# Optimization experiments

Hardware: AMD Instinct MI355X
Metric: run time of the kernel (lower is better)

## Reference

```python
import jax, jax.numpy as jnp
import numpy as np

N = 50000   # num_nodes
F = 128     # node_features
E = 800000  # num_edges (avg degree 16)


def setup_inputs() -> dict:
    key = jax.random.key(0)
    ks = jax.random.split(key, 12)
    s = 1.0 / np.sqrt(F)
    return {
        "x": jax.random.normal(ks[0], (N, F), jnp.float32),
        "edge_index": jax.random.randint(ks[1], (2, E), 0, N),
        "edge_weight": jax.random.uniform(ks[2], (E,), jnp.float32),
        # TopKPooling projection vector p (PyG stores it as [1, F])
        "p": jax.random.normal(ks[3], (F,), jnp.float32) * s,
        # GRU params, torch gate order (r, z, n)
        "w_ih": jax.random.normal(ks[4], (3 * F, F), jnp.float32) * s,
        "w_hh": jax.random.normal(ks[5], (3 * F, F), jnp.float32) * s,
        "b_ih": jax.random.normal(ks[6], (3 * F,), jnp.float32) * s,
        "b_hh": jax.random.normal(ks[7], (3 * F,), jnp.float32) * s,
        # initial evolving GCN weight [F, F] (glorot-initialized in original)
        "W0": jax.random.normal(ks[8], (F, F), jnp.float32) * s,
        # trailing Linear(F, F)
        "W_lin": jax.random.normal(ks[9], (F, F), jnp.float32) * s,
        "b_lin": jax.random.normal(ks[10], (F,), jnp.float32) * s,
    }


def reference(x, edge_index, edge_weight, p, w_ih, w_hh, b_ih, b_hh, W0, W_lin, b_lin):
    n_nodes, f = x.shape
    # --- TopKPooling: score nodes, select top-F (ratio = F/N) ---
    score = jnp.tanh((x @ p) / jnp.linalg.norm(p))          # [N]
    top_scores, perm = jax.lax.top_k(score, f)              # sorted desc, k = F
    x_tilde = x[perm] * top_scores[:, None]                 # [F, F]
    # --- GRU single step (seq_len=1, batch=F): evolve weight matrix ---
    gi = x_tilde @ w_ih.T + b_ih                            # [F, 3F]
    gh = W0 @ w_hh.T + b_hh                                 # [F, 3F]
    r = jax.nn.sigmoid(gi[:, :f] + gh[:, :f])
    z = jax.nn.sigmoid(gi[:, f:2 * f] + gh[:, f:2 * f])
    n = jnp.tanh(gi[:, 2 * f:] + r * gh[:, 2 * f:])
    W = (1.0 - z) * n + z * W0                              # evolved [F, F]
    # --- GCNConv_Fixed_W: gcn_norm (self-loops, sym norm) + aggregate ---
    loop = jnp.arange(n_nodes)
    row = jnp.concatenate([edge_index[0], loop])            # sources
    col = jnp.concatenate([edge_index[1], loop])            # targets
    ew = jnp.concatenate([edge_weight, jnp.ones((n_nodes,), x.dtype)])
    deg = jax.ops.segment_sum(ew, col, num_segments=n_nodes)
    dinv = jnp.where(deg > 0, jnp.where(deg > 0, deg, 1.0) ** -0.5, 0.0)
    norm = dinv[row] * ew * dinv[col]                       # [E+N]
    xw = x @ W                                              # [N, F]
    h = jax.ops.segment_sum(norm[:, None] * xw[row], col, num_segments=n_nodes)
    # --- relu + Linear ---
    return jax.nn.relu(h) @ W_lin.T + b_lin
```

## Files before the change

### kernel.cpp

```cpp
#include <hip/hip_runtime.h>
#include <hip/hip_fp16.h>

#define NF 128
#define TK 128

typedef _Float16 f16;
typedef f16 half8 __attribute__((ext_vector_type(8)));
typedef float floatx4 __attribute__((ext_vector_type(4)));

__device__ __forceinline__ unsigned okey(float f) {
  unsigned u = __float_as_uint(f);
  return (u & 0x80000000u) ? ~u : (u | 0x80000000u);
}

__global__ void score_hist_kernel(const float* __restrict__ x, const float* __restrict__ p,
                                  float* __restrict__ score, unsigned* __restrict__ keys,
                                  unsigned* __restrict__ bins, const int* __restrict__ ei,
                                  const float* __restrict__ ew,
                                  unsigned long long* __restrict__ cnt64,
                                  unsigned short* __restrict__ eslot, int n, int E, int nbScore) {
  if ((int)blockIdx.x >= nbScore) {
    int e = ((int)blockIdx.x - nbScore) * 256 + threadIdx.x;
    if (e < E) {
      int c = ei[E + e];
      unsigned fx = __float2uint_rn(ew[e] * 16777216.0f);
      unsigned long long old =
          atomicAdd(&cnt64[c], ((unsigned long long)1 << 32) | (unsigned long long)fx);
      eslot[e] = (unsigned short)(old >> 32);
    }
    return;
  }
  int wib = threadIdx.x >> 6, lane = threadIdx.x & 63;
  int r = blockIdx.x * 4 + wib;
  if (r >= n) return;
  float2 xv = *(const float2*)&x[(size_t)r * NF + lane * 2];
  float2 pv = *(const float2*)&p[lane * 2];
  float d = fmaf(xv.x, pv.x, xv.y * pv.y);
  float pp = fmaf(pv.x, pv.x, pv.y * pv.y);
#pragma unroll
  for (int off = 32; off > 0; off >>= 1) {
    d += __shfl_down(d, off, 64);
    pp += __shfl_down(pp, off, 64);
  }
  if (lane == 0) {
    float s = tanhf(d / sqrtf(pp));
    score[r] = s;
    unsigned k = okey(s);
    keys[r] = k;
    atomicAdd(&bins[k >> 16], 1u);
  }
}

__global__ __launch_bounds__(1024) void findbin_kernel(const unsigned* __restrict__ bins,
                                                       unsigned* __restrict__ thrB) {
  __shared__ unsigned csum[1024];
  int t = threadIdx.x;
  unsigned hv[64];
  unsigned s = 0;
  const unsigned* bp = bins + t * 64;
#pragma unroll
  for (int b = 0; b < 64; ++b) { hv[b] = bp[b]; s += hv[b]; }
  csum[t] = s;
  __syncthreads();
  for (int st = 1; st < 1024; st <<= 1) {
    unsigned add = (t + st < 1024) ? csum[t + st] : 0u;
    __syncthreads();
    csum[t] += add;
    __syncthreads();
  }
  unsigned mySum = csum[t];
  unsigned above = (t == 1023) ? 0u : csum[t + 1];
  if (mySum >= (unsigned)TK && above < (unsigned)TK) {
    unsigned cum = above;
    int b = 63;
    for (; b > 0; --b) {
      unsigned h = hv[b];
      if (cum + h >= (unsigned)TK) break;
      cum += h;
    }
    thrB[0] = (unsigned)(t * 64 + b);
  }
}

#define SCAN_B 1024
__global__ __launch_bounds__(1024) void scan1_kernel(const unsigned long long* __restrict__ cnt64,
                                                     int* __restrict__ offL, int* __restrict__ bsum,
                                                     float* __restrict__ dinv,
                                                     const unsigned* __restrict__ keys,
                                                     const unsigned* __restrict__ thrB,
                                                     int* __restrict__ ncnt,
                                                     int* __restrict__ candIdx, int n) {
  __shared__ int sd[SCAN_B];
  int t = threadIdx.x;
  int i = blockIdx.x * SCAN_B + t;
  int v = 0;
  if (i < n) {
    unsigned long long cv = cnt64[i];
    v = (int)(cv >> 32);
    float dsum = (float)((unsigned)cv) * (1.0f / 16777216.0f) + 1.0f;
    dinv[i] = 1.0f / sqrtf(dsum);
    if ((keys[i] >> 16) >= thrB[0]) {
      int pos = atomicAdd(ncnt, 1);
      candIdx[pos] = i;
    }
  }
  sd[t] = v;
  __syncthreads();
  for (int s = 1; s < SCAN_B; s <<= 1) {
    int add = (t >= s) ? sd[t - s] : 0;
    __syncthreads();
    sd[t] += add;
    __syncthreads();
  }
  if (i <= n) offL[i] = sd[t] - v;
  if (t == SCAN_B - 1) bsum[blockIdx.x] = sd[t];
}

#define CCAP 6144
__global__ __launch_bounds__(1024) void scan2_select_kernel(const int* __restrict__ bsum,
                                                            int* __restrict__ bexc, int nb,
                                                            const unsigned* __restrict__ keys,
                                                            const int* __restrict__ candIdx,
                                                            const int* __restrict__ ncp,
                                                            const float* __restrict__ score,
                                                            int* __restrict__ perm,
                                                            float* __restrict__ tsc) {
  if (blockIdx.x == 0) {
    int t = threadIdx.x;
    if (t < 64) {
      int v = (t < nb) ? bsum[t] : 0;
      int incl = v;
#pragma unroll
      for (int s = 1; s < 64; s <<= 1) {
        int u = __shfl_up(incl, s, 64);
        if (t >= s) incl += u;
      }
      if (t <= nb) bexc[t] = incl - v;
    }
    return;
  }
  __shared__ unsigned sk[CCAP];
  __shared__ int si[CCAP];
  int nc = ncp[0];
  int t = threadIdx.x;
  int m = nc < CCAP ? nc : CCAP;
  for (int i = t; i < m; i += 1024) {
    int ci = candIdx[i];
    si[i] = ci;
    sk[i] = keys[ci];
  }
  __syncthreads();
  for (int ci = t; ci < nc; ci += 1024) {
    unsigned mk;
    int mi;
    if (ci < CCAP) { mk = sk[ci]; mi = si[ci]; }
    else { mi = candIdx[ci]; mk = keys[mi]; }
    int rank = 0;
    for (int j = 0; j < m; ++j) {
      unsigned kj = sk[j];
      int ij = si[j];
      rank += (kj > mk || (kj == mk && ij < mi)) ? 1 : 0;
    }
    for (int j = CCAP; j < nc; ++j) {
      int ij = candIdx[j];
      unsigned kj = keys[ij];
      rank += (kj > mk || (kj == mk && ij < mi)) ? 1 : 0;
    }
    if (rank < TK) {
      perm[rank] = mi;
      tsc[rank] = score[mi];
    }
  }
}

__global__ void gru_kernel(const float* __restrict__ x, const int* __restrict__ perm,
                           const float* __restrict__ tsc, const float* __restrict__ W0,
                           const float* __restrict__ w_ih, const float* __restrict__ w_hh,
                           const float* __restrict__ b_ih, const float* __restrict__ b_hh,
                           float* __restrict__ WT) {
  __shared__ float xs[NF], w0s[NF];
  int i = blockIdx.x, j = threadIdx.x;
  int pi = perm[i];
  float s = tsc[i];
  xs[j] = x[(size_t)pi * NF + j] * s;
  w0s[j] = W0[i * NF + j];
  __syncthreads();
  float gir = b_ih[j], giz = b_ih[NF + j], gin = b_ih[2 * NF + j];
  float ghr = b_hh[j], ghz = b_hh[NF + j], ghn = b_hh[2 * NF + j];
  const float* wr = w_ih + (size_t)j * NF;
  const float* wz = w_ih + (size_t)(NF + j) * NF;
  const float* wn = w_ih + (size_t)(2 * NF + j) * NF;
  const float* ur = w_hh + (size_t)j * NF;
  const float* uz = w_hh + (size_t)(NF + j) * NF;
  const float* un = w_hh + (size_t)(2 * NF + j) * NF;
#pragma unroll 4
  for (int k = 0; k < NF; ++k) {
    float xv = xs[k], wv = w0s[k];
    gir = fmaf(xv, wr[k], gir);
    giz = fmaf(xv, wz[k], giz);
    gin = fmaf(xv, wn[k], gin);
    ghr = fmaf(wv, ur[k], ghr);
    ghz = fmaf(wv, uz[k], ghz);
    ghn = fmaf(wv, un[k], ghn);
  }
  float r = 1.0f / (1.0f + expf(-(gir + ghr)));
  float z = 1.0f / (1.0f + expf(-(giz + ghz)));
  float nn = tanhf(gin + r * ghn);
  WT[(size_t)j * NF + i] = (1.0f - z) * nn + z * w0s[j];
}

__global__ void fill_kernel(const int* __restrict__ ei, const float* __restrict__ ew,
                            const float* __restrict__ dinv, const int* __restrict__ offL,
                            const int* __restrict__ bexc, const unsigned short* __restrict__ eslot,
                            unsigned* __restrict__ epair, int E) {
  int e = blockIdx.x * 256 + threadIdx.x;
  if (e >= E) return;
  int r = ei[e], c = ei[E + e];
  int pos = offL[c] + bexc[c >> 10] + (int)eslot[e];
  float cf = dinv[r] * ew[e] * dinv[c];
  unsigned hb = (unsigned)__builtin_bit_cast(unsigned short, __float2half(cf));
  epair[pos] = (unsigned)r | (hb << 16);
}

__global__ void aggregate_kernel(const unsigned* __restrict__ epair, const int* __restrict__ offL,
                                 const int* __restrict__ bexc, const float* __restrict__ dinv,
                                 const uint4* __restrict__ xw4, unsigned* __restrict__ hh, int n) {
  int w = (int)((blockIdx.x * (size_t)blockDim.x + threadIdx.x) >> 6);
  if (w >= n) return;
  int lane = threadIdx.x & 63;
  int q = lane >> 4, l16 = lane & 15;
  int n0 = offL[w] + bexc[w >> 10];
  int n1 = offL[w + 1] + bexc[(w + 1) >> 10];
  float acc[8] = {0.f, 0.f, 0.f, 0.f, 0.f, 0.f, 0.f, 0.f};
  if (q == 0) {
    float dv = dinv[w];
    float c2 = dv * dv;
    uint4 su = xw4[(size_t)w * 16 + l16];
    float2 f0 = __half22float2(*(const __half2*)&su.x);
    float2 f1 = __half22float2(*(const __half2*)&su.y);
    float2 f2 = __half22float2(*(const __half2*)&su.z);
    float2 f3 = __half22float2(*(const __half2*)&su.w);
    acc[0] = c2 * f0.x; acc[1] = c2 * f0.y; acc[2] = c2 * f1.x; acc[3] = c2 * f1.y;
    acc[4] = c2 * f2.x; acc[5] = c2 * f2.y; acc[6] = c2 * f3.x; acc[7] = c2 * f3.y;
  }
  int e = n0 + q;
  for (; e + 4 < n1; e += 8) {
    unsigned p0 = epair[e], p1 = epair[e + 4];
    uint4 u0 = xw4[(size_t)(p0 & 0xFFFFu) * 16 + l16];
    uint4 u1 = xw4[(size_t)(p1 & 0xFFFFu) * 16 + l16];
    float c0 = __half2float(__builtin_bit_cast(__half, (unsigned short)(p0 >> 16)));
    float c1 = __half2float(__builtin_bit_cast(__half, (unsigned short)(p1 >> 16)));
    float2 f0, f1, f2, f3;
    f0 = __half22float2(*(const __half2*)&u0.x); f1 = __half22float2(*(const __half2*)&u0.y);
    f2 = __half22float2(*(const __half2*)&u0.z); f3 = __half22float2(*(const __half2*)&u0.w);
    acc[0] = fmaf(c0, f0.x, acc[0]); acc[1] = fmaf(c0, f0.y, acc[1]);
    acc[2] = fmaf(c0, f1.x, acc[2]); acc[3] = fmaf(c0, f1.y, acc[3]);
    acc[4] = fmaf(c0, f2.x, acc[4]); acc[5] = fmaf(c0, f2.y, acc[5]);
    acc[6] = fmaf(c0, f3.x, acc[6]); acc[7] = fmaf(c0, f3.y, acc[7]);
    f0 = __half22float2(*(const __half2*)&u1.x); f1 = __half22float2(*(const __half2*)&u1.y);
    f2 = __half22float2(*(const __half2*)&u1.z); f3 = __half22float2(*(const __half2*)&u1.w);
    acc[0] = fmaf(c1, f0.x, acc[0]); acc[1] = fmaf(c1, f0.y, acc[1]);
    acc[2] = fmaf(c1, f1.x, acc[2]); acc[3] = fmaf(c1, f1.y, acc[3]);
    acc[4] = fmaf(c1, f2.x, acc[4]); acc[5] = fmaf(c1, f2.y, acc[5]);
    acc[6] = fmaf(c1, f3.x, acc[6]); acc[7] = fmaf(c1, f3.y, acc[7]);
  }
  for (; e < n1; e += 4) {
    unsigned p0 = epair[e];
    uint4 u0 = xw4[(size_t)(p0 & 0xFFFFu) * 16 + l16];
    float c0 = __half2float(__builtin_bit_cast(__half, (unsigned short)(p0 >> 16)));
    float2 f0 = __half22float2(*(const __half2*)&u0.x);
    float2 f1 = __half22float2(*(const __half2*)&u0.y);
    float2 f2 = __half22float2(*(const __half2*)&u0.z);
    float2 f3 = __half22float2(*(const __half2*)&u0.w);
    acc[0] = fmaf(c0, f0.x, acc[0]); acc[1] = fmaf(c0, f0.y, acc[1]);
    acc[2] = fmaf(c0, f1.x, acc[2]); acc[3] = fmaf(c0, f1.y, acc[3]);
    acc[4] = fmaf(c0, f2.x, acc[4]); acc[5] = fmaf(c0, f2.y, acc[5]);
    acc[6] = fmaf(c0, f3.x, acc[6]); acc[7] = fmaf(c0, f3.y, acc[7]);
  }
#pragma unroll
  for (int j = 0; j < 8; ++j) {
    float a = acc[j];
    a += __shfl_xor(a, 16, 64);
    a += __shfl_xor(a, 32, 64);
    acc[j] = a;
  }
  if (q == 0) {
    __half2 h0 = __floats2half2_rn(fmaxf(acc[0], 0.f), fmaxf(acc[1], 0.f));
    __half2 h1 = __floats2half2_rn(fmaxf(acc[2], 0.f), fmaxf(acc[3], 0.f));
    __half2 h2 = __floats2half2_rn(fmaxf(acc[4], 0.f), fmaxf(acc[5], 0.f));
    __half2 h3 = __floats2half2_rn(fmaxf(acc[6], 0.f), fmaxf(acc[7], 0.f));
    uint4 o;
    o.x = *(unsigned*)&h0; o.y = *(unsigned*)&h1; o.z = *(unsigned*)&h2; o.w = *(unsigned*)&h3;
    *(uint4*)&hh[(size_t)w * 64 + l16 * 4] = o;
  }
}

template <int HIN, int HOUT, int BIAS>
__global__ __launch_bounds__(256) void gemm_mfma_kernel(const void* __restrict__ Ap,
                                                        const float* __restrict__ Bt,
                                                        const float* __restrict__ bias,
                                                        void* __restrict__ Cp, int nrows) {
  __shared__ char ldsA[64 * 256];
  __shared__ char ldsB[128 * 256];
  const int t = threadIdx.x;
  const int row0 = blockIdx.x * 64;
  {
    const float2* B2 = (const float2*)Bt;
#pragma unroll
    for (int i = 0; i < 32; ++i) {
      int idx = i * 256 + t;
      int nn = idx >> 6, kp = idx & 63;
      float2 v = B2[idx];
      __half2 h = __floats2half2_rn(v.x, v.y);
      int byte = (nn * 256 + kp * 4) ^ ((nn & 7) << 4);
      *(unsigned*)&ldsB[byte] = *(unsigned*)&h;
    }
  }
  if (HIN) {
    const unsigned* Ah = (const unsigned*)Ap;
#pragma unroll
    for (int i = 0; i < 16; ++i) {
      int idx = i * 256 + t;
      int r = idx >> 6, cp = idx & 63;
      int gr = row0 + r;
      unsigned v = (gr < nrows) ? Ah[(size_t)gr * 64 + cp] : 0u;
      int byte = (r * 256 + cp * 4) ^ ((r & 7) << 4);
      *(unsigned*)&ldsA[byte] = v;
    }
  } else {
    const float2* A2 = (const float2*)Ap;
#pragma unroll
    for (int i = 0; i < 16; ++i) {
      int idx = i * 256 + t;
      int r = idx >> 6, cp = idx & 63;
      int gr = row0 + r;
      float2 v = make_float2(0.f, 0.f);
      if (gr < nrows) v = A2[(size_t)gr * 64 + cp];
      __half2 h = __floats2half2_rn(v.x, v.y);
      int byte = (r * 256 + cp * 4) ^ ((r & 7) << 4);
      *(unsigned*)&ldsA[byte] = *(unsigned*)&h;
    }
  }
  __syncthreads();
  const int wave = t >> 6, l = t & 63;
  const int wr0 = wave * 16;
  const int lm = l & 15, q = l >> 4;
  floatx4 acc[8];
#pragma unroll
  for (int nt = 0; nt < 8; ++nt) acc[nt] = (floatx4){0.f, 0.f, 0.f, 0.f};
#pragma unroll
  for (int ks = 0; ks < 4; ++ks) {
    int arow = wr0 + lm;
    half8 a = *(const half8*)&ldsA[(arow * 256 + ks * 64 + q * 16) ^ ((arow & 7) << 4)];
#pragma unroll
    for (int nt = 0; nt < 8; ++nt) {
      int nn = nt * 16 + lm;
      half8 b = *(const half8*)&ldsB[(nn * 256 + ks * 64 + q * 16) ^ ((nn & 7) << 4)];
      acc[nt] = __builtin_amdgcn_mfma_f32_16x16x32_f16(a, b, acc[nt], 0, 0, 0);
    }
  }
#pragma unroll
  for (int nt = 0; nt < 8; ++nt) {
    int col = nt * 16 + lm;
    float bv = BIAS ? bias[col] : 0.f;
#pragma unroll
    for (int r = 0; r < 4; ++r) {
      int gr = row0 + wr0 + q * 4 + r;
      if (gr < nrows) {
        float v = acc[nt][r] + bv;
        if (HOUT) ((__half*)Cp)[(size_t)gr * NF + col] = __float2half(v);
        else ((float*)Cp)[(size_t)gr * NF + col] = v;
      }
    }
  }
}

extern "C" void kernel_launch(void* const* d_in, const int* in_sizes, int n_in,
                              void* d_out, int out_size, void* d_ws, size_t ws_size,
                              hipStream_t stream) {
  const float* x = (const float*)d_in[0];
  const int* ei = (const int*)d_in[1];
  const float* ew = (const float*)d_in[2];
  const float* p = (const float*)d_in[3];
  const float* w_ih = (const float*)d_in[4];
  const float* w_hh = (const float*)d_in[5];
  const float* b_ih = (const float*)d_in[6];
  const float* b_hh = (const float*)d_in[7];
  const float* W0 = (const float*)d_in[8];
  const float* W_lin = (const float*)d_in[9];
  const float* b_lin = (const float*)d_in[10];
  float* out = (float*)d_out;

  const int N = in_sizes[0] / NF;
  const int E = in_sizes[1] / 2;

  char* w = (char*)d_ws;
  unsigned* xwh = (unsigned*)w;
  unsigned* hh = xwh + (size_t)N * 64;
  float* score = (float*)(hh + (size_t)N * 64);
  unsigned* keys = (unsigned*)(score + N);
  unsigned long long* cnt64 = (unsigned long long*)(keys + N);
  unsigned* bins = (unsigned*)(cnt64 + N);
  int* ncnt = (int*)(bins + 65536);
  float* dinv = (float*)(ncnt + 1);
  unsigned* thrB = (unsigned*)(dinv + N);
  int* candIdx = (int*)(thrB + 1);
  int* offL = candIdx + N;
  int* bsum = offL + N + 1;
  int* bexc = bsum + 64;
  unsigned short* eslot = (unsigned short*)(bexc + 64);
  unsigned* epair = (unsigned*)(eslot + E);
  float* WevT = (float*)(epair + E);
  int* perm = (int*)(WevT + NF * NF);
  float* tsc = (float*)(perm + NF);

  const int nb = (N + SCAN_B - 1) / SCAN_B;
  const int nbScore = (N + 3) / 4;
  const int nbEdge = (E + 255) / 256;
  const int nbGemm = (N + 63) / 64;

  hipMemsetAsync(cnt64, 0, (size_t)N * 8 + 65536 * 4 + 4, stream);
  score_hist_kernel<<<nbScore + nbEdge, 256, 0, stream>>>(x, p, score, keys, bins, ei, ew,
                                                          cnt64, eslot, N, E, nbScore);
  findbin_kernel<<<1, 1024, 0, stream>>>(bins, thrB);
  scan1_kernel<<<nb, SCAN_B, 0, stream>>>(cnt64, offL, bsum, dinv, keys, thrB, ncnt,
                                          candIdx, N);
  scan2_select_kernel<<<2, 1024, 0, stream>>>(bsum, bexc, nb, keys, candIdx, ncnt, score,
                                              perm, tsc);
  gru_kernel<<<NF, NF, 0, stream>>>(x, perm, tsc, W0, w_ih, w_hh, b_ih, b_hh, WevT);
  fill_kernel<<<nbEdge, 256, 0, stream>>>(ei, ew, dinv, offL, bexc, eslot, epair, E);
  gemm_mfma_kernel<0, 1, 0><<<nbGemm, 256, 0, stream>>>(x, WevT, nullptr, xwh, N);
  aggregate_kernel<<<(N + 3) / 4, 256, 0, stream>>>(epair, offL, bexc, dinv,
                                                    (const uint4*)xwh, hh, N);
  gemm_mfma_kernel<1, 0, 1><<<nbGemm, 256, 0, stream>>>(hh, W_lin, b_lin, out, N);
}
```

Measured before the change: 220.0 us.

## Spread edge degree counting across the serial top-k and GRU kernels

The edge-degree atomic counting used to be fused into the score kernel. It is now split into four slices that ride as extra blocks on findbin, compaction, selection and GRU, which are small latency-bound launches that leave most of the GPU idle. The scan, which needs the finished counts, moves after the first GEMM, and compaction is separated from the scan. This aims to fill idle compute units during the serial top-k chain. In exchange, the extra blocks may slow those critical-path kernels and add another launch (scan2).

```diff
diff --git a/kernel.cpp b/kernel.cpp
--- a/kernel.cpp
+++ b/kernel.cpp
@@ -13,23 +13,21 @@
   return (u & 0x80000000u) ? ~u : (u | 0x80000000u);
 }
 
-__global__ void score_hist_kernel(const float* __restrict__ x, const float* __restrict__ p,
-                                  float* __restrict__ score, unsigned* __restrict__ keys,
-                                  unsigned* __restrict__ bins, const int* __restrict__ ei,
-                                  const float* __restrict__ ew,
-                                  unsigned long long* __restrict__ cnt64,
-                                  unsigned short* __restrict__ eslot, int n, int E, int nbScore) {
-  if ((int)blockIdx.x >= nbScore) {
-    int e = ((int)blockIdx.x - nbScore) * 256 + threadIdx.x;
-    if (e < E) {
-      int c = ei[E + e];
-      unsigned fx = __float2uint_rn(ew[e] * 16777216.0f);
-      unsigned long long old =
-          atomicAdd(&cnt64[c], ((unsigned long long)1 << 32) | (unsigned long long)fx);
-      eslot[e] = (unsigned short)(old >> 32);
-    }
-    return;
-  }
+__device__ __forceinline__ void edge_slice(const int* __restrict__ ei, const float* __restrict__ ew,
+                                           unsigned long long* __restrict__ cnt64,
+                                           unsigned short* __restrict__ eslot, int E, int e, int elim) {
+  if (e < elim) {
+    int c = ei[E + e];
+    unsigned fx = __float2uint_rn(ew[e] * 16777216.0f);
+    unsigned long long old =
+        atomicAdd(&cnt64[c], ((unsigned long long)1 << 32) | (unsigned long long)fx);
+    eslot[e] = (unsigned short)(old >> 32);
+  }
+}
+
+__global__ void score_kernel(const float* __restrict__ x, const float* __restrict__ p,
+                             float* __restrict__ score, unsigned* __restrict__ keys,
+                             unsigned* __restrict__ bins, int n) {
   int wib = threadIdx.x >> 6, lane = threadIdx.x & 63;
   int r = blockIdx.x * 4 + wib;
   if (r >= n) return;
@@ -51,8 +49,17 @@
   }
 }
 
-__global__ __launch_bounds__(1024) void findbin_kernel(const unsigned* __restrict__ bins,
-                                                       unsigned* __restrict__ thrB) {
+__global__ __launch_bounds__(1024) void findbin_edge_kernel(const unsigned* __restrict__ bins,
+                                                            unsigned* __restrict__ thrB,
+                                                            const int* __restrict__ ei,
+                                                            const float* __restrict__ ew,
+                                                            unsigned long long* __restrict__ cnt64,
+                                                            unsigned short* __restrict__ eslot,
+                                                            int E, int ebase, int elim) {
+  if (blockIdx.x > 0) {
+    edge_slice(ei, ew, cnt64, eslot, E, ebase + ((int)blockIdx.x - 1) * 1024 + (int)threadIdx.x, elim);
+    return;
+  }
   __shared__ unsigned csum[1024];
   int t = threadIdx.x;
   unsigned hv[64];
@@ -82,61 +89,43 @@
   }
 }
 
-#define SCAN_B 1024
-__global__ __launch_bounds__(1024) void scan1_kernel(const unsigned long long* __restrict__ cnt64,
-                                                     int* __restrict__ offL, int* __restrict__ bsum,
-                                                     float* __restrict__ dinv,
-                                                     const unsigned* __restrict__ keys,
-                                                     const unsigned* __restrict__ thrB,
-                                                     int* __restrict__ ncnt,
-                                                     int* __restrict__ candIdx, int n) {
-  __shared__ int sd[SCAN_B];
-  int t = threadIdx.x;
-  int i = blockIdx.x * SCAN_B + t;
-  int v = 0;
+__global__ __launch_bounds__(1024) void compact_edge_kernel(const unsigned* __restrict__ keys,
+                                                            const unsigned* __restrict__ thrB,
+                                                            int* __restrict__ ncnt,
+                                                            int* __restrict__ candIdx, int n, int nOwn,
+                                                            const int* __restrict__ ei,
+                                                            const float* __restrict__ ew,
+                                                            unsigned long long* __restrict__ cnt64,
+                                                            unsigned short* __restrict__ eslot,
+                                                            int E, int ebase, int elim) {
+  if ((int)blockIdx.x >= nOwn) {
+    edge_slice(ei, ew, cnt64, eslot, E,
+               ebase + ((int)blockIdx.x - nOwn) * 1024 + (int)threadIdx.x, elim);
+    return;
+  }
+  int i = blockIdx.x * 1024 + threadIdx.x;
   if (i < n) {
-    unsigned long long cv = cnt64[i];
-    v = (int)(cv >> 32);
-    float dsum = (float)((unsigned)cv) * (1.0f / 16777216.0f) + 1.0f;
-    dinv[i] = 1.0f / sqrtf(dsum);
     if ((keys[i] >> 16) >= thrB[0]) {
       int pos = atomicAdd(ncnt, 1);
       candIdx[pos] = i;
     }
   }
-  sd[t] = v;
-  __syncthreads();
-  for (int s = 1; s < SCAN_B; s <<= 1) {
-    int add = (t >= s) ? sd[t - s] : 0;
-    __syncthreads();
-    sd[t] += add;
-    __syncthreads();
-  }
-  if (i <= n) offL[i] = sd[t] - v;
-  if (t == SCAN_B - 1) bsum[blockIdx.x] = sd[t];
 }
 
 #define CCAP 6144
-__global__ __launch_bounds__(1024) void scan2_select_kernel(const int* __restrict__ bsum,
-                                                            int* __restrict__ bexc, int nb,
-                                                            const unsigned* __restrict__ keys,
-                                                            const int* __restrict__ candIdx,
-                                                            const int* __restrict__ ncp,
-                                                            const float* __restrict__ score,
-                                                            int* __restrict__ perm,
-                                                            float* __restrict__ tsc) {
-  if (blockIdx.x == 0) {
-    int t = threadIdx.x;
-    if (t < 64) {
-      int v = (t < nb) ? bsum[t] : 0;
-      int incl = v;
-#pragma unroll
-      for (int s = 1; s < 64; s <<= 1) {
-        int u = __shfl_up(incl, s, 64);
-        if (t >= s) incl += u;
-      }
-      if (t <= nb) bexc[t] = incl - v;
-    }
+__global__ __launch_bounds__(1024) void select_edge_kernel(const unsigned* __restrict__ keys,
+                                                           const int* __restrict__ candIdx,
+                                                           const int* __restrict__ ncp,
+                                                           const float* __restrict__ score,
+                                                           int* __restrict__ perm,
+                                                           float* __restrict__ tsc,
+                                                           const int* __restrict__ ei,
+                                                           const float* __restrict__ ew,
+                                                           unsigned long long* __restrict__ cnt64,
+                                                           unsigned short* __restrict__ eslot,
+                                                           int E, int ebase, int elim) {
+  if (blockIdx.x > 0) {
+    edge_slice(ei, ew, cnt64, eslot, E, ebase + ((int)blockIdx.x - 1) * 1024 + (int)threadIdx.x, elim);
     return;
   }
   __shared__ unsigned sk[CCAP];
@@ -173,11 +162,18 @@
   }
 }
 
-__global__ void gru_kernel(const float* __restrict__ x, const int* __restrict__ perm,
-                           const float* __restrict__ tsc, const float* __restrict__ W0,
-                           const float* __restrict__ w_ih, const float* __restrict__ w_hh,
-                           const float* __restrict__ b_ih, const float* __restrict__ b_hh,
-                           float* __restrict__ WT) {
+__global__ void gru_edge_kernel(const float* __restrict__ x, const int* __restrict__ perm,
+                                const float* __restrict__ tsc, const float* __restrict__ W0,
+                                const float* __restrict__ w_ih, const float* __restrict__ w_hh,
+                                const float* __restrict__ b_ih, const float* __restrict__ b_hh,
+                                float* __restrict__ WT,
+                                const int* __restrict__ ei, const float* __restrict__ ew,
+                                unsigned long long* __restrict__ cnt64,
+                                unsigned short* __restrict__ eslot, int E, int ebase, int elim) {
+  if ((int)blockIdx.x >= NF) {
+    edge_slice(ei, ew, cnt64, eslot, E, ebase + ((int)blockIdx.x - NF) * 128 + (int)threadIdx.x, elim);
+    return;
+  }
   __shared__ float xs[NF], w0s[NF];
   int i = blockIdx.x, j = threadIdx.x;
   int pi = perm[i];
@@ -209,6 +205,46 @@
   WT[(size_t)j * NF + i] = (1.0f - z) * nn + z * w0s[j];
 }
 
+#define SCAN_B 1024
+__global__ __launch_bounds__(1024) void scan1_kernel(const unsigned long long* __restrict__ cnt64,
+                                                     int* __restrict__ offL, int* __restrict__ bsum,
+                                                     float* __restrict__ dinv, int n) {
+  __shared__ int sd[SCAN_B];
+  int t = threadIdx.x;
+  int i = blockIdx.x * SCAN_B + t;
+  int v = 0;
+  if (i < n) {
+    unsigned long long cv = cnt64[i];
+    v = (int)(cv >> 32);
+    float dsum = (float)((unsigned)cv) * (1.0f / 16777216.0f) + 1.0f;
+    dinv[i] = 1.0f / sqrtf(dsum);
+  }
+  sd[t] = v;
+  __syncthreads();
+  for (int s = 1; s < SCAN_B; s <<= 1) {
+    int add = (t >= s) ? sd[t - s] : 0;
+    __syncthreads();
+    sd[t] += add;
+    __syncthreads();
+  }
+  if (i <= n) offL[i] = sd[t] - v;
+  if (t == SCAN_B - 1) bsum[blockIdx.x] = sd[t];
+}
+
+__global__ void scan2_kernel(const int* __restrict__ bsum, int* __restrict__ bexc, int nb) {
+  int t = threadIdx.x;
+  if (t < 64) {
+    int v = (t < nb) ? bsum[t] : 0;
+    int incl = v;
+#pragma unroll
+    for (int s = 1; s < 64; s <<= 1) {
+      int u = __shfl_up(incl, s, 64);
+      if (t >= s) incl += u;
+    }
+    if (t <= nb) bexc[t] = incl - v;
+  }
+}
+
 __global__ void fill_kernel(const int* __restrict__ ei, const float* __restrict__ ew,
                             const float* __restrict__ dinv, const int* __restrict__ offL,
                             const int* __restrict__ bexc, const unsigned short* __restrict__ eslot,
@@ -415,21 +451,33 @@
   float* tsc = (float*)(perm + NF);
 
   const int nb = (N + SCAN_B - 1) / SCAN_B;
-  const int nbScore = (N + 3) / 4;
   const int nbEdge = (E + 255) / 256;
   const int nbGemm = (N + 63) / 64;
+  const int nOwnC = (N + 1023) / 1024;
+
+  const int per = (E + 3) / 4;
+  const int bA = (per + 1023) / 1024;
+  const int eA0 = 0, eA1 = (bA * 1024 < E) ? bA * 1024 : E;
+  const int bB = (per + 1023) / 1024;
+  const int eB0 = eA1, eB1 = (eB0 + bB * 1024 < E) ? eB0 + bB * 1024 : E;
+  const int bC = (per + 1023) / 1024;
+  const int eC0 = eB1, eC1 = (eC0 + bC * 1024 < E) ? eC0 + bC * 1024 : E;
+  const int eD0 = eC1;
+  const int bD = (E - eD0 + 127) / 128;
 
   hipMemsetAsync(cnt64, 0, (size_t)N * 8 + 65536 * 4 + 4, stream);
-  score_hist_kernel<<<nbScore + nbEdge, 256, 0, stream>>>(x, p, score, keys, bins, ei, ew,
-                                                          cnt64, eslot, N, E, nbScore);
-  findbin_kernel<<<1, 1024, 0, stream>>>(bins, thrB);
-  scan1_kernel<<<nb, SCAN_B, 0, stream>>>(cnt64, offL, bsum, dinv, keys, thrB, ncnt,
-                                          candIdx, N);
-  scan2_select_kernel<<<2, 1024, 0, stream>>>(bsum, bexc, nb, keys, candIdx, ncnt, score,
-                                              perm, tsc);
-  gru_kernel<<<NF, NF, 0, stream>>>(x, perm, tsc, W0, w_ih, w_hh, b_ih, b_hh, WevT);
+  score_kernel<<<(N + 3) / 4, 256, 0, stream>>>(x, p, score, keys, bins, N);
+  findbin_edge_kernel<<<1 + bA, 1024, 0, stream>>>(bins, thrB, ei, ew, cnt64, eslot, E, eA0, eA1);
+  compact_edge_kernel<<<nOwnC + bB, 1024, 0, stream>>>(keys, thrB, ncnt, candIdx, N, nOwnC,
+                                                       ei, ew, cnt64, eslot, E, eB0, eB1);
+  select_edge_kernel<<<1 + bC, 1024, 0, stream>>>(keys, candIdx, ncnt, score, perm, tsc,
+                                                  ei, ew, cnt64, eslot, E, eC0, eC1);
+  gru_edge_kernel<<<NF + bD, NF, 0, stream>>>(x, perm, tsc, W0, w_ih, w_hh, b_ih, b_hh, WevT,
+                                              ei, ew, cnt64, eslot, E, eD0, E);
+  gemm_mfma_kernel<0, 1, 0><<<nbGemm, 256, 0, stream>>>(x, WevT, nullptr, xwh, N);
+  scan1_kernel<<<nb, SCAN_B, 0, stream>>>(cnt64, offL, bsum, dinv, N);
+  scan2_kernel<<<1, 64, 0, stream>>>(bsum, bexc, nb);
   fill_kernel<<<nbEdge, 256, 0, stream>>>(ei, ew, dinv, offL, bexc, eslot, epair, E);
-  gemm_mfma_kernel<0, 1, 0><<<nbGemm, 256, 0, stream>>>(x, WevT, nullptr, xwh, N);
   aggregate_kernel<<<(N + 3) / 4, 256, 0, stream>>>(epair, offL, bexc, dinv,
                                                     (const uint4*)xwh, hh, N);
   gemm_mfma_kernel<1, 0, 1><<<nbGemm, 256, 0, stream>>>(hh, W_lin, b_lin, out, N);
```

After: 217.9 us. No clear change (-1.0%).
